# Performance work log

Measured on AMD Instinct MI355X. Metric: run time of the kernel, lower is better.

Reference implementation:

```python
import jax, jax.numpy as jnp
import numpy as np

HIDDEN = 1024
N_HEADS = 16
HEAD_DIM = HIDDEN // N_HEADS
B, S = 4, 2048


def setup_inputs() -> dict:
    key = jax.random.key(0)
    ks = jax.random.split(key, 11)
    init = lambda k, shape: jax.random.normal(k, shape, dtype=jnp.float32) * (1.0 / np.sqrt(shape[0]))
    return {
        "query": jax.random.normal(ks[0], (B, S, HIDDEN), dtype=jnp.float32),
        "key": jax.random.normal(ks[1], (B, S, HIDDEN), dtype=jnp.float32),
        "value": jax.random.normal(ks[2], (B, S, HIDDEN), dtype=jnp.float32),
        "Wq": init(ks[3], (HIDDEN, HIDDEN)), "bq": jnp.zeros((HIDDEN,), jnp.float32),
        "Wk": init(ks[4], (HIDDEN, HIDDEN)), "bk": jnp.zeros((HIDDEN,), jnp.float32),
        "Wv": init(ks[5], (HIDDEN, HIDDEN)), "bv": jnp.zeros((HIDDEN,), jnp.float32),
        "Wo": init(ks[6], (HIDDEN, HIDDEN)), "bo": jnp.zeros((HIDDEN,), jnp.float32),
    }


def reference(query, key, value, Wq, bq, Wk, bk, Wv, bv, Wo, bo):
    b, s, h = query.shape
    # QKV projections
    Q = query @ Wq + bq
    K = key @ Wk + bk
    V = value @ Wv + bv
    # split heads: [B, H, S, D]
    Q = Q.reshape(b, s, N_HEADS, HEAD_DIM).transpose(0, 2, 1, 3)
    K = K.reshape(b, s, N_HEADS, HEAD_DIM).transpose(0, 2, 1, 3)
    V = V.reshape(b, s, N_HEADS, HEAD_DIM).transpose(0, 2, 1, 3)
    scale = jnp.sqrt(jnp.asarray(HEAD_DIM, query.dtype))
    # scores: [B, H, S, S]
    scores = jnp.einsum("bhqd,bhkd->bhqk", Q, K) / scale
    attn = jax.nn.softmax(scores, axis=-1)
    out = jnp.einsum("bhqk,bhkd->bhqd", attn, V)
    out = out.transpose(0, 2, 1, 3).reshape(b, s, h)
    return out @ Wo + bo
```

## Files before the change

### kernel.cpp

```cpp
#include <hip/hip_runtime.h>
#include <hip/hip_bf16.h>

#define HID 1024
#define NH 16
#define HD 64
#define SEQ 2048
#define MTOT 8192
#define QSCALE 0.18033688011112042f

typedef __bf16 bf16x8 __attribute__((ext_vector_type(8)));
typedef float f32x4 __attribute__((ext_vector_type(4)));

static __device__ __forceinline__ float fast_exp2(float x) {
#if __has_builtin(__builtin_amdgcn_exp2f)
    return __builtin_amdgcn_exp2f(x);
#else
    return __expf(x * 0.6931471805599453f);
#endif
}

static __device__ __forceinline__ unsigned short bfbits(float f) {
    __bf16 b = (__bf16)f;
    return __builtin_bit_cast(unsigned short, b);
}

static __device__ __forceinline__ bf16x8 frag16(const unsigned short* p) {
    return __builtin_bit_cast(bf16x8, *(const uint4*)p);
}

__global__ void wt_kernel(const float* __restrict__ W, unsigned short* __restrict__ Wt) {
    __shared__ float tile[32][33];
    const int n0 = blockIdx.x * 32, k0 = blockIdx.y * 32;
    const int tx = threadIdx.x, ty = threadIdx.y;
#pragma unroll
    for (int i = 0; i < 4; ++i)
        tile[ty + i * 8][tx] = W[(size_t)(k0 + ty + i * 8) * HID + n0 + tx];
    __syncthreads();
#pragma unroll
    for (int i = 0; i < 4; ++i)
        Wt[(size_t)(n0 + ty + i * 8) * HID + k0 + tx] = bfbits(tile[tx][ty + i * 8]);
}

template <int AMODE, int OMODE>
__global__ __launch_bounds__(256, 2) void gemm_kernel(
    const void* __restrict__ Av, const unsigned short* __restrict__ Bt,
    const float* __restrict__ bias, void* __restrict__ Cv, const float sc) {
    __shared__ unsigned short smA[128][40];
    __shared__ unsigned short smB[128][40];
    const int tid = threadIdx.x;
    const int lane = tid & 63;
    const int wid = tid >> 6, wr = wid >> 1, wc = wid & 1;
    const int lr = lane & 15, lk = lane >> 4;
    const int m0 = blockIdx.x * 128, n0 = blockIdx.y * 128;
    const int srow = tid >> 1, skh = (tid & 1) * 16;

    f32x4 acc[4][4] = {};

    for (int kt = 0; kt < HID / 32; ++kt) {
        const int k0 = kt * 32;
        __syncthreads();
        if (AMODE == 0) {
            const float* src = (const float*)Av + (size_t)(m0 + srow) * HID + k0 + skh;
            float4 a0 = *(const float4*)(src);
            float4 a1 = *(const float4*)(src + 4);
            float4 a2 = *(const float4*)(src + 8);
            float4 a3 = *(const float4*)(src + 12);
            union { __bf16 h[8]; uint4 v; } u0, u1;
            u0.h[0] = (__bf16)a0.x; u0.h[1] = (__bf16)a0.y; u0.h[2] = (__bf16)a0.z; u0.h[3] = (__bf16)a0.w;
            u0.h[4] = (__bf16)a1.x; u0.h[5] = (__bf16)a1.y; u0.h[6] = (__bf16)a1.z; u0.h[7] = (__bf16)a1.w;
            u1.h[0] = (__bf16)a2.x; u1.h[1] = (__bf16)a2.y; u1.h[2] = (__bf16)a2.z; u1.h[3] = (__bf16)a2.w;
            u1.h[4] = (__bf16)a3.x; u1.h[5] = (__bf16)a3.y; u1.h[6] = (__bf16)a3.z; u1.h[7] = (__bf16)a3.w;
            *(uint4*)&smA[srow][skh] = u0.v;
            *(uint4*)&smA[srow][skh + 8] = u1.v;
        } else {
            const unsigned short* src = (const unsigned short*)Av + (size_t)(m0 + srow) * HID + k0 + skh;
            *(uint4*)&smA[srow][skh] = *(const uint4*)(src);
            *(uint4*)&smA[srow][skh + 8] = *(const uint4*)(src + 8);
        }
        {
            const unsigned short* src = Bt + (size_t)(n0 + srow) * HID + k0 + skh;
            *(uint4*)&smB[srow][skh] = *(const uint4*)(src);
            *(uint4*)&smB[srow][skh + 8] = *(const uint4*)(src + 8);
        }
        __syncthreads();
        bf16x8 af[4], bfr[4];
#pragma unroll
        for (int m = 0; m < 4; ++m) af[m] = frag16(&smA[wr * 64 + m * 16 + lr][lk * 8]);
#pragma unroll
        for (int n = 0; n < 4; ++n) bfr[n] = frag16(&smB[wc * 64 + n * 16 + lr][lk * 8]);
#pragma unroll
        for (int m = 0; m < 4; ++m)
#pragma unroll
            for (int n = 0; n < 4; ++n)
                acc[m][n] = __builtin_amdgcn_mfma_f32_16x16x32_bf16(af[m], bfr[n], acc[m][n], 0, 0, 0);
    }

#pragma unroll
    for (int m = 0; m < 4; ++m) {
#pragma unroll
        for (int n = 0; n < 4; ++n) {
            const int col = n0 + wc * 64 + n * 16 + lr;
            const float bv = bias[col];
            const int row0 = m0 + wr * 64 + m * 16 + lk * 4;
            if (OMODE == 2) {
                const int b = row0 >> 11, s0 = row0 & 2047;
                const int h = col >> 6, d = col & 63;
                unsigned short* dst = (unsigned short*)Cv +
                    ((((size_t)b * NH + h) * HD + d) * SEQ + s0);
                uint2 pk;
                pk.x = (unsigned)bfbits((acc[m][n][0] + bv) * sc) |
                       ((unsigned)bfbits((acc[m][n][1] + bv) * sc) << 16);
                pk.y = (unsigned)bfbits((acc[m][n][2] + bv) * sc) |
                       ((unsigned)bfbits((acc[m][n][3] + bv) * sc) << 16);
                *(uint2*)dst = pk;
            } else {
#pragma unroll
                for (int j = 0; j < 4; ++j) {
                    const int row = row0 + j;
                    const float v = (acc[m][n][j] + bv) * sc;
                    if (OMODE == 0) {
                        ((float*)Cv)[(size_t)row * HID + col] = v;
                    } else {
                        const int b = row >> 11, s = row & 2047;
                        const int h = col >> 6, d = col & 63;
                        ((unsigned short*)Cv)[((((size_t)b * NH + h) * SEQ + s) << 6) + d] = bfbits(v);
                    }
                }
            }
        }
    }
}

__global__ __launch_bounds__(256, 4) void flash_kernel(
    const unsigned short* __restrict__ Q, const unsigned short* __restrict__ K,
    const unsigned short* __restrict__ Vt, unsigned short* __restrict__ O) {
    __shared__ unsigned short smK[64][72];
    __shared__ unsigned short smV[64][72];
    __shared__ unsigned short smP[4][32][72];

    const int tid = threadIdx.x;
    const int lane = tid & 63, w = tid >> 6;
    const int lr = lane & 15, lk = lane >> 4;

    const int L = blockIdx.y * 16 + blockIdx.x;
    const int xcd = L & 7, slot = L >> 3;
    const int bh = xcd + 8 * (slot >> 4);
    const int qt = slot & 15;

    const int b = bh >> 4, h = bh & 15;
    const int q0 = qt * 128 + w * 32;

    const unsigned short* Qb = Q + (size_t)bh * SEQ * HD;
    const unsigned short* Kb = K + (size_t)bh * SEQ * HD;
    const unsigned short* Vb = Vt + (size_t)bh * HD * SEQ;

    bf16x8 qf[2][2];
#pragma unroll
    for (int m = 0; m < 2; ++m)
#pragma unroll
        for (int kk = 0; kk < 2; ++kk)
            qf[m][kk] = frag16(&Qb[(size_t)(q0 + m * 16 + lr) * HD + kk * 32 + lk * 8]);

    f32x4 accO[2][4] = {};
    float lsum[2] = {0.f, 0.f};

    const int srow = tid >> 2, sseg = (tid & 3) * 16;
    const unsigned short* Kp = Kb + (size_t)srow * HD + sseg;
    const unsigned short* Vp = Vb + (size_t)srow * SEQ + sseg;

    uint4 kr0, kr1, vr0, vr1;
    kr0 = *(const uint4*)Kp; kr1 = *(const uint4*)(Kp + 8);
    vr0 = *(const uint4*)Vp; vr1 = *(const uint4*)(Vp + 8);
    *(uint4*)&smK[srow][sseg] = kr0; *(uint4*)&smK[srow][sseg + 8] = kr1;
    *(uint4*)&smV[srow][sseg] = vr0; *(uint4*)&smV[srow][sseg + 8] = vr1;
    __syncthreads();

    const int NT = SEQ / 64;
    for (int kt = 0; kt < NT; ++kt) {
        if (kt + 1 < NT) {
            const unsigned short* kp = Kp + (size_t)(kt + 1) * 64 * HD;
            const unsigned short* vp = Vp + (kt + 1) * 64;
            kr0 = *(const uint4*)kp; kr1 = *(const uint4*)(kp + 8);
            vr0 = *(const uint4*)vp; vr1 = *(const uint4*)(vp + 8);
        }

        f32x4 s[2][4] = {};
#pragma unroll
        for (int kk = 0; kk < 2; ++kk) {
            bf16x8 kf[4];
#pragma unroll
            for (int n = 0; n < 4; ++n) kf[n] = frag16(&smK[n * 16 + lr][kk * 32 + lk * 8]);
#pragma unroll
            for (int m = 0; m < 2; ++m)
#pragma unroll
                for (int n = 0; n < 4; ++n)
                    s[m][n] = __builtin_amdgcn_mfma_f32_16x16x32_bf16(kf[n], qf[m][kk], s[m][n], 0, 0, 0);
        }

#pragma unroll
        for (int m = 0; m < 2; ++m) {
            float rs = 0.f;
#pragma unroll
            for (int n = 0; n < 4; ++n) {
                union { __bf16 hh[4]; uint2 v; } u;
#pragma unroll
                for (int j = 0; j < 4; ++j) {
                    const float p = fast_exp2(s[m][n][j]);
                    rs += p;
                    u.hh[j] = (__bf16)p;
                }
                *(uint2*)&smP[w][m * 16 + lr][n * 16 + lk * 4] = u.v;
            }
            lsum[m] += rs;
        }

#pragma unroll
        for (int ks = 0; ks < 2; ++ks) {
            bf16x8 pf[2], vf[4];
#pragma unroll
            for (int m = 0; m < 2; ++m) pf[m] = frag16(&smP[w][m * 16 + lr][ks * 32 + lk * 8]);
#pragma unroll
            for (int n = 0; n < 4; ++n) vf[n] = frag16(&smV[n * 16 + lr][ks * 32 + lk * 8]);
#pragma unroll
            for (int m = 0; m < 2; ++m)
#pragma unroll
                for (int n = 0; n < 4; ++n)
                    accO[m][n] = __builtin_amdgcn_mfma_f32_16x16x32_bf16(pf[m], vf[n], accO[m][n], 0, 0, 0);
        }
        __syncthreads();
        if (kt + 1 < NT) {
            *(uint4*)&smK[srow][sseg] = kr0; *(uint4*)&smK[srow][sseg + 8] = kr1;
            *(uint4*)&smV[srow][sseg] = vr0; *(uint4*)&smV[srow][sseg + 8] = vr1;
        }
        __syncthreads();
    }

#pragma unroll
    for (int m = 0; m < 2; ++m) {
        float t = lsum[m];
        t += __shfl_xor(t, 16);
        t += __shfl_xor(t, 32);
        const float invl = 1.0f / t;
#pragma unroll
        for (int j = 0; j < 4; ++j) {
            const float inv = __shfl(invl, lk * 4 + j);
            const int sg = q0 + m * 16 + lk * 4 + j;
#pragma unroll
            for (int n = 0; n < 4; ++n) {
                const int d = n * 16 + lr;
                O[((size_t)b * SEQ + sg) * HID + h * HD + d] = bfbits(accO[m][n][j] * inv);
            }
        }
    }
}

extern "C" void kernel_launch(void* const* d_in, const int* in_sizes, int n_in,
                              void* d_out, int out_size, void* d_ws, size_t ws_size,
                              hipStream_t stream) {
    const float* q  = (const float*)d_in[0];
    const float* k  = (const float*)d_in[1];
    const float* v  = (const float*)d_in[2];
    const float* Wq = (const float*)d_in[3]; const float* bq = (const float*)d_in[4];
    const float* Wk = (const float*)d_in[5]; const float* bk = (const float*)d_in[6];
    const float* Wv = (const float*)d_in[7]; const float* bv = (const float*)d_in[8];
    const float* Wo = (const float*)d_in[9]; const float* bo = (const float*)d_in[10];
    float* out = (float*)d_out;

    unsigned short* Wtq = (unsigned short*)d_ws;
    unsigned short* Wtk = Wtq + (size_t)HID * HID;
    unsigned short* Wtv = Wtk + (size_t)HID * HID;
    unsigned short* Wto = Wtv + (size_t)HID * HID;
    unsigned short* Qb  = Wto + (size_t)HID * HID;
    unsigned short* Kb  = Qb + (size_t)MTOT * HID;
    unsigned short* Vtb = Kb + (size_t)MTOT * HID;
    unsigned short* Ob  = Vtb + (size_t)MTOT * HID;

    dim3 tb(32, 8);
    wt_kernel<<<dim3(32, 32), tb, 0, stream>>>(Wq, Wtq);
    wt_kernel<<<dim3(32, 32), tb, 0, stream>>>(Wk, Wtk);
    wt_kernel<<<dim3(32, 32), tb, 0, stream>>>(Wv, Wtv);
    wt_kernel<<<dim3(32, 32), tb, 0, stream>>>(Wo, Wto);

    gemm_kernel<0, 1><<<dim3(64, 8), 256, 0, stream>>>(q, Wtq, bq, Qb, QSCALE);
    gemm_kernel<0, 1><<<dim3(64, 8), 256, 0, stream>>>(k, Wtk, bk, Kb, 1.0f);
    gemm_kernel<0, 2><<<dim3(64, 8), 256, 0, stream>>>(v, Wtv, bv, Vtb, 1.0f);

    flash_kernel<<<dim3(16, 64), 256, 0, stream>>>(Qb, Kb, Vtb, Ob);

    gemm_kernel<1, 0><<<dim3(64, 8), 256, 0, stream>>>(Ob, Wto, bo, out, 1.0f);
}
```

Before: 233.3 us.

## Register-prefetch GEMM tiles with K=64 steps and merge weight transpose launches

The GEMM main loop now moves to 64-wide K tiles and prefetches the next tile from global memory into registers while MFMAs run on the current shared-memory tile. This overlaps global load latency with compute and halves the number of barrier pairs per K sweep. The four weight-transpose launches are merged into one 3D-grid launch to cut launch overhead. The cost is more registers for the prefetch buffers, especially in the fp32 A path, and larger shared-memory tiles, which could hurt occupancy under the 2-blocks-per-SM launch bound.

```diff
diff --git a/kernel.cpp b/kernel.cpp
--- a/kernel.cpp
+++ b/kernel.cpp
@@ -28,8 +28,14 @@
     return __builtin_bit_cast(bf16x8, *(const uint4*)p);
 }
 
-__global__ void wt_kernel(const float* __restrict__ W, unsigned short* __restrict__ Wt) {
+__global__ void wt4_kernel(const float* __restrict__ W0, const float* __restrict__ W1,
+                           const float* __restrict__ W2, const float* __restrict__ W3,
+                           unsigned short* __restrict__ T0, unsigned short* __restrict__ T1,
+                           unsigned short* __restrict__ T2, unsigned short* __restrict__ T3) {
     __shared__ float tile[32][33];
+    const int z = blockIdx.z;
+    const float* W = (z == 0) ? W0 : (z == 1) ? W1 : (z == 2) ? W2 : W3;
+    unsigned short* Wt = (z == 0) ? T0 : (z == 1) ? T1 : (z == 2) ? T2 : T3;
     const int n0 = blockIdx.x * 32, k0 = blockIdx.y * 32;
     const int tx = threadIdx.x, ty = threadIdx.y;
 #pragma unroll
@@ -45,54 +51,81 @@
 __global__ __launch_bounds__(256, 2) void gemm_kernel(
     const void* __restrict__ Av, const unsigned short* __restrict__ Bt,
     const float* __restrict__ bias, void* __restrict__ Cv, const float sc) {
-    __shared__ unsigned short smA[128][40];
-    __shared__ unsigned short smB[128][40];
+    __shared__ unsigned short smA[128][72];
+    __shared__ unsigned short smB[128][72];
     const int tid = threadIdx.x;
     const int lane = tid & 63;
-    const int wid = tid >> 6, wr = wid >> 1, wc = wid & 1;
+    const int w = tid >> 6, wr = w >> 1, wc = w & 1;
     const int lr = lane & 15, lk = lane >> 4;
     const int m0 = blockIdx.x * 128, n0 = blockIdx.y * 128;
-    const int srow = tid >> 1, skh = (tid & 1) * 16;
+
+    const int srow = tid >> 1;
+    const int shalf = (tid & 1) * 32;
 
     f32x4 acc[4][4] = {};
-
-    for (int kt = 0; kt < HID / 32; ++kt) {
-        const int k0 = kt * 32;
+    float4 pa[8];
+    uint4 pa16[4];
+    uint4 pb[4];
+
+    auto loadT = [&](int kt) {
+        const int k0 = kt * 64;
+        if (AMODE == 0) {
+            const float* src = (const float*)Av + (size_t)(m0 + srow) * HID + k0 + shalf;
+#pragma unroll
+            for (int i = 0; i < 8; ++i) pa[i] = *(const float4*)(src + i * 4);
+        } else {
+            const unsigned short* src = (const unsigned short*)Av + (size_t)(m0 + srow) * HID + k0 + shalf;
+#pragma unroll
+            for (int i = 0; i < 4; ++i) pa16[i] = *((const uint4*)src + i);
+        }
+        const unsigned short* srcB = Bt + (size_t)(n0 + srow) * HID + k0 + shalf;
+#pragma unroll
+        for (int i = 0; i < 4; ++i) pb[i] = *((const uint4*)srcB + i);
+    };
+
+    auto writeT = [&]() {
+        if (AMODE == 0) {
+#pragma unroll
+            for (int p = 0; p < 4; ++p) {
+                union { __bf16 h[8]; uint4 v; } u;
+                u.h[0] = (__bf16)pa[2 * p].x; u.h[1] = (__bf16)pa[2 * p].y;
+                u.h[2] = (__bf16)pa[2 * p].z; u.h[3] = (__bf16)pa[2 * p].w;
+                u.h[4] = (__bf16)pa[2 * p + 1].x; u.h[5] = (__bf16)pa[2 * p + 1].y;
+                u.h[6] = (__bf16)pa[2 * p + 1].z; u.h[7] = (__bf16)pa[2 * p + 1].w;
+                *(uint4*)&smA[srow][shalf + p * 8] = u.v;
+            }
+        } else {
+#pragma unroll
+            for (int p = 0; p < 4; ++p)
+                *(uint4*)&smA[srow][shalf + p * 8] = pa16[p];
+        }
+#pragma unroll
+        for (int p = 0; p < 4; ++p)
+            *(uint4*)&smB[srow][shalf + p * 8] = pb[p];
+    };
+
+    const int kIters = HID / 64;
+    loadT(0);
+    for (int kt = 0; kt < kIters; ++kt) {
         __syncthreads();
-        if (AMODE == 0) {
-            const float* src = (const float*)Av + (size_t)(m0 + srow) * HID + k0 + skh;
-            float4 a0 = *(const float4*)(src);
-            float4 a1 = *(const float4*)(src + 4);
-            float4 a2 = *(const float4*)(src + 8);
-            float4 a3 = *(const float4*)(src + 12);
-            union { __bf16 h[8]; uint4 v; } u0, u1;
-            u0.h[0] = (__bf16)a0.x; u0.h[1] = (__bf16)a0.y; u0.h[2] = (__bf16)a0.z; u0.h[3] = (__bf16)a0.w;
-            u0.h[4] = (__bf16)a1.x; u0.h[5] = (__bf16)a1.y; u0.h[6] = (__bf16)a1.z; u0.h[7] = (__bf16)a1.w;
-            u1.h[0] = (__bf16)a2.x; u1.h[1] = (__bf16)a2.y; u1.h[2] = (__bf16)a2.z; u1.h[3] = (__bf16)a2.w;
-            u1.h[4] = (__bf16)a3.x; u1.h[5] = (__bf16)a3.y; u1.h[6] = (__bf16)a3.z; u1.h[7] = (__bf16)a3.w;
-            *(uint4*)&smA[srow][skh] = u0.v;
-            *(uint4*)&smA[srow][skh + 8] = u1.v;
-        } else {
-            const unsigned short* src = (const unsigned short*)Av + (size_t)(m0 + srow) * HID + k0 + skh;
-            *(uint4*)&smA[srow][skh] = *(const uint4*)(src);
-            *(uint4*)&smA[srow][skh + 8] = *(const uint4*)(src + 8);
-        }
-        {
-            const unsigned short* src = Bt + (size_t)(n0 + srow) * HID + k0 + skh;
-            *(uint4*)&smB[srow][skh] = *(const uint4*)(src);
-            *(uint4*)&smB[srow][skh + 8] = *(const uint4*)(src + 8);
-        }
+        writeT();
         __syncthreads();
-        bf16x8 af[4], bfr[4];
-#pragma unroll
-        for (int m = 0; m < 4; ++m) af[m] = frag16(&smA[wr * 64 + m * 16 + lr][lk * 8]);
-#pragma unroll
-        for (int n = 0; n < 4; ++n) bfr[n] = frag16(&smB[wc * 64 + n * 16 + lr][lk * 8]);
-#pragma unroll
-        for (int m = 0; m < 4; ++m)
+        if (kt + 1 < kIters) loadT(kt + 1);
+#pragma unroll
+        for (int kk = 0; kk < 2; ++kk) {
+            bf16x8 af[4], bfr[4];
+#pragma unroll
+            for (int m = 0; m < 4; ++m)
+                af[m] = frag16(&smA[wr * 64 + m * 16 + lr][kk * 32 + lk * 8]);
 #pragma unroll
             for (int n = 0; n < 4; ++n)
-                acc[m][n] = __builtin_amdgcn_mfma_f32_16x16x32_bf16(af[m], bfr[n], acc[m][n], 0, 0, 0);
+                bfr[n] = frag16(&smB[wc * 64 + n * 16 + lr][kk * 32 + lk * 8]);
+#pragma unroll
+            for (int m = 0; m < 4; ++m)
+#pragma unroll
+                for (int n = 0; n < 4; ++n)
+                    acc[m][n] = __builtin_amdgcn_mfma_f32_16x16x32_bf16(af[m], bfr[n], acc[m][n], 0, 0, 0);
+        }
     }
 
 #pragma unroll
@@ -275,11 +308,8 @@
     unsigned short* Vtb = Kb + (size_t)MTOT * HID;
     unsigned short* Ob  = Vtb + (size_t)MTOT * HID;
 
-    dim3 tb(32, 8);
-    wt_kernel<<<dim3(32, 32), tb, 0, stream>>>(Wq, Wtq);
-    wt_kernel<<<dim3(32, 32), tb, 0, stream>>>(Wk, Wtk);
-    wt_kernel<<<dim3(32, 32), tb, 0, stream>>>(Wv, Wtv);
-    wt_kernel<<<dim3(32, 32), tb, 0, stream>>>(Wo, Wto);
+    wt4_kernel<<<dim3(32, 32, 4), dim3(32, 8), 0, stream>>>(
+        Wq, Wk, Wv, Wo, Wtq, Wtk, Wtv, Wto);
 
     gemm_kernel<0, 1><<<dim3(64, 8), 256, 0, stream>>>(q, Wtq, bq, Qb, QSCALE);
     gemm_kernel<0, 1><<<dim3(64, 8), 256, 0, stream>>>(k, Wtk, bk, Kb, 1.0f);
```

Result: slower. 392.1 us (+68.1%).
